# Optimization experiments

Hardware: AMD Instinct MI355X
Metric: run time of the kernel (lower is better)

## Reference

```python
import jax, jax.numpy as jnp
import numpy as np

N_NODES = 100000
N_EDGES = 1600000
NUM_FEATURES = 64
HIDDEN = 64
NUM_CLASSES = 16


def setup_inputs() -> dict:
    key = jax.random.key(0)
    ks = jax.random.split(key, 8)
    x = jax.random.normal(ks[0], (N_NODES, NUM_FEATURES), dtype=jnp.float32)
    edge_index = jax.random.randint(ks[1], (2, N_EDGES), 0, N_NODES, dtype=jnp.int32)
    # Glorot-ish init for weights, zero bias (matches GCNConv / Linear defaults closely enough)
    s1 = 1.0 / np.sqrt(NUM_FEATURES)
    s2 = 1.0 / np.sqrt(HIDDEN)
    W1 = jax.random.uniform(ks[2], (NUM_FEATURES, HIDDEN), jnp.float32, -s1, s1)
    b1 = jnp.zeros((HIDDEN,), jnp.float32)
    W2 = jax.random.uniform(ks[3], (HIDDEN, HIDDEN), jnp.float32, -s2, s2)
    b2 = jnp.zeros((HIDDEN,), jnp.float32)
    W3 = jax.random.uniform(ks[4], (HIDDEN, NUM_CLASSES), jnp.float32, -s2, s2)
    b3 = jax.random.uniform(ks[5], (NUM_CLASSES,), jnp.float32, -s2, s2)
    return {"x": x, "edge_index": edge_index, "W1": W1, "b1": b1,
            "W2": W2, "b2": b2, "W3": W3, "b3": b3}


def _gcn_layer(x, W, b, src, dst, norm, n_nodes):
    # GCNConv: h = X W; out[i] = sum_{(j->i)} norm_ji * h[j]; out += b
    h = x @ W                                   # [N, H] small dense GEMM
    msg = h[src] * norm[:, None]                # [E+N, H] irregular gather
    out = jax.ops.segment_sum(msg, dst, num_segments=n_nodes)  # scatter-add
    return out + b


def reference(x, edge_index, W1, b1, W2, b2, W3, b3):
    n = x.shape[0]
    loop = jnp.arange(n, dtype=edge_index.dtype)
    # add self-loops (PyG GCNConv default add_self_loops=True)
    src = jnp.concatenate([edge_index[0], loop])
    dst = jnp.concatenate([edge_index[1], loop])
    # symmetric normalization D^{-1/2} A_hat D^{-1/2}
    deg = jax.ops.segment_sum(jnp.ones_like(src, dtype=x.dtype), dst, num_segments=n)
    dis = jax.lax.rsqrt(deg)                    # deg >= 1 due to self-loops
    norm = dis[src] * dis[dst]                  # [E+N]

    h = jax.nn.relu(_gcn_layer(x, W1, b1, src, dst, norm, n))
    # F.dropout(training=False) -> identity (module in eval mode)
    h = jax.nn.relu(_gcn_layer(h, W2, b2, src, dst, norm, n))
    z = h @ W3 + b3
    return jax.nn.log_softmax(z, axis=1), h
```

## Files before the change

### kernel.cpp

```cpp
#include <hip/hip_runtime.h>
#include <hip/hip_bf16.h>

typedef __hip_bfloat16 bf16;
typedef unsigned short ushort;

#define NN 100000
#define NE 1600000
#define NBKT 782
#define BCAP 4096
#define EPB 2048
#define NP1 782
#define NMT 6250

typedef __attribute__((ext_vector_type(8))) short s8v;
typedef __attribute__((ext_vector_type(4))) float f4v;

__device__ __forceinline__ float ldf(const void* p, int i, int f32) {
    return f32 ? ((const float*)p)[i] : __bfloat162float(((const bf16*)p)[i]);
}
__device__ __forceinline__ void stf(void* p, int i, int f32, float v) {
    if (f32) ((float*)p)[i] = v;
    else     ((bf16*)p)[i] = __float2bfloat16(v);
}

__device__ __forceinline__ ushort f2b(float f) {
    unsigned u = __builtin_bit_cast(unsigned, f);
    u += 0x7FFF + ((u >> 16) & 1);
    return (ushort)(u >> 16);
}
__device__ __forceinline__ float b2f(ushort h) {
    unsigned u = ((unsigned)h) << 16;
    return __builtin_bit_cast(float, u);
}
__device__ __forceinline__ float blo(unsigned u) {
    return __builtin_bit_cast(float, u << 16);
}
__device__ __forceinline__ float bhi(unsigned u) {
    return __builtin_bit_cast(float, u & 0xffff0000u);
}

__global__ void k_detect(const unsigned* __restrict__ x, int* __restrict__ flag,
                         int* __restrict__ gcur) {
    int gi = blockIdx.x * 256 + threadIdx.x;
    if (gi < 1024) gcur[gi] = 0;
    if (blockIdx.x != 0) return;
    __shared__ int cnt[256];
    int t = threadIdx.x, c = 0;
    for (int i = t; i < 2048; i += 256) {
        unsigned e7 = (x[i] >> 8) & 0x7F;
        c += (e7 >= 60 && e7 <= 66) ? 1 : 0;
    }
    cnt[t] = c;
    __syncthreads();
    for (int s = 128; s > 0; s >>= 1) {
        if (t < s) cnt[t] += cnt[t + s];
        __syncthreads();
    }
    if (t == 0) *flag = (cnt[0] >= 1024) ? 0 : 1;
}

__global__ void k_sentinel(unsigned* out) {
    if (threadIdx.x == 0 && blockIdx.x == 0) out[0] = 0x461C461Cu;
}

__global__ void k_pass1(const int* __restrict__ src, const int* __restrict__ dst,
                        int* __restrict__ gcur, unsigned* __restrict__ bbuf) {
    __shared__ int hist[NBKT];
    __shared__ int base[NBKT];
    int t = threadIdx.x;
    int e0 = blockIdx.x * EPB;
    for (int i = t; i < NBKT; i += 256) hist[i] = 0;
    __syncthreads();
    for (int k = 0; k < EPB; k += 256) {
        int e = e0 + k + t;
        if (e < NE) atomicAdd(&hist[dst[e] >> 7], 1);
    }
    __syncthreads();
    for (int i = t; i < NBKT; i += 256) {
        int c = hist[i];
        base[i] = c ? atomicAdd(&gcur[i], c) : 0;
    }
    __syncthreads();
    for (int i = t; i < NBKT; i += 256) hist[i] = 0;
    __syncthreads();
    for (int k = 0; k < EPB; k += 256) {
        int e = e0 + k + t;
        if (e < NE) {
            int d = dst[e];
            int b = d >> 7;
            int lp = atomicAdd(&hist[b], 1);
            bbuf[b * BCAP + base[b] + lp] = ((unsigned)src[e] << 7) | (unsigned)(d & 127);
        }
    }
}

__global__ void k_scanB(const int* __restrict__ gcur, int* __restrict__ gbase,
                        int* __restrict__ rowptr) {
    __shared__ int s[1024];
    int t = threadIdx.x;
    int v = (t < NBKT) ? gcur[t] : 0;
    s[t] = v;
    __syncthreads();
    for (int d = 1; d < 1024; d <<= 1) {
        int add = (t >= d) ? s[t - d] : 0;
        __syncthreads();
        s[t] += add;
        __syncthreads();
    }
    if (t < NBKT) gbase[t] = s[t] - v;
    if (t == 0) { gbase[NBKT] = NE; rowptr[NN] = NE; }
}

__global__ void k_pass2(const unsigned* __restrict__ bbuf, const int* __restrict__ gbase,
                        int* __restrict__ rowptr, float* __restrict__ dis,
                        int* __restrict__ csr_off) {
    __shared__ unsigned vals[BCAP];
    __shared__ int lout[BCAP];
    __shared__ int fh[128], fx[128], fc[128];
    int b = blockIdx.x, t = threadIdx.x;
    int g0 = gbase[b], cnt = gbase[b + 1] - g0;
    const unsigned* in = bbuf + b * BCAP;
    if (t < 128) fh[t] = 0;
    __syncthreads();
    for (int i = t; i < cnt; i += 256) {
        unsigned v = in[i];
        vals[i] = v;
        atomicAdd(&fh[v & 127], 1);
    }
    __syncthreads();
    if (t < 128) fx[t] = fh[t];
    __syncthreads();
    for (int d = 1; d < 128; d <<= 1) {
        int add = (t >= d && t < 128) ? fx[t - d] : 0;
        __syncthreads();
        if (t < 128) fx[t] += add;
        __syncthreads();
    }
    int n = b * 128 + t;
    if (t < 128) {
        int ex = fx[t] - fh[t];
        fc[t] = ex;
        if (n < NN) {
            rowptr[n] = g0 + ex;
            dis[n] = rsqrtf(1.0f + (float)fh[t]);
        }
    }
    __syncthreads();
    for (int i = t; i < cnt; i += 256) {
        unsigned v = vals[i];
        int p = atomicAdd(&fc[v & 127], 1);
        lout[p] = (int)(v & ~127u);
    }
    __syncthreads();
    for (int i = t; i < cnt; i += 256) csr_off[g0 + i] = lout[i];
}

__global__ void __launch_bounds__(256) k_gemm_mfma(
        const void* __restrict__ A, int aBase, const void* __restrict__ W,
        bf16* __restrict__ C, const float* __restrict__ dis,
        const int* __restrict__ flag) {
    int f32 = *flag;
    int t = threadIdx.x;
    if (blockIdx.x == 0 && t < 64) ((ushort*)C)[NN * 64 + t] = 0;
    int lane = t & 63;
    int w = t >> 6;
    int m = lane & 15, q = lane >> 4;

    s8v bh[2][4], bl[2][4];
#pragma unroll
    for (int st = 0; st < 2; st++)
#pragma unroll
        for (int nt = 0; nt < 4; nt++)
#pragma unroll
            for (int j = 0; j < 8; j++) {
                int k = st * 32 + q * 8 + j;
                float wv = ldf(W, k * 64 + nt * 16 + m, f32);
                ushort h = f2b(wv);
                bh[st][nt][j] = (short)h;
                bl[st][nt][j] = (short)f2b(wv - b2f(h));
            }

    ushort* Cu = (ushort*)C;
    int gw = blockIdx.x * 4 + w;
    int nw = gridDim.x * 4;
    for (int mt = gw; mt < NMT; mt += nw) {
        int row = mt * 16 + m;
        s8v ah[2], al[2];
        if (f32) {
            const float* ap = (const float*)A + aBase + row * 64 + q * 8;
#pragma unroll
            for (int st = 0; st < 2; st++)
#pragma unroll
                for (int j = 0; j < 8; j++) {
                    float v = ap[st * 32 + j];
                    ushort h = f2b(v);
                    ah[st][j] = (short)h;
                    al[st][j] = (short)f2b(v - b2f(h));
                }
        } else {
            const short* ap = (const short*)A + aBase + row * 64 + q * 8;
            ah[0] = *(const s8v*)(ap);
            ah[1] = *(const s8v*)(ap + 32);
        }
        float dr[4];
#pragma unroll
        for (int r = 0; r < 4; r++) dr[r] = dis[mt * 16 + q * 4 + r];
#pragma unroll
        for (int nt = 0; nt < 4; nt++) {
            f4v acc = {0.f, 0.f, 0.f, 0.f};
#pragma unroll
            for (int st = 0; st < 2; st++)
                acc = __builtin_amdgcn_mfma_f32_16x16x32_bf16(ah[st], bh[st][nt], acc, 0, 0, 0);
            if (f32) {
#pragma unroll
                for (int st = 0; st < 2; st++) {
                    acc = __builtin_amdgcn_mfma_f32_16x16x32_bf16(ah[st], bl[st][nt], acc, 0, 0, 0);
                    acc = __builtin_amdgcn_mfma_f32_16x16x32_bf16(al[st], bh[st][nt], acc, 0, 0, 0);
                }
            }
            int col = nt * 16 + m;
#pragma unroll
            for (int r = 0; r < 4; r++) {
                int rr = mt * 16 + q * 4 + r;
                Cu[rr * 64 + col] = f2b(dr[r] * acc[r]);
            }
        }
    }
}

__global__ void __launch_bounds__(256, 4) k_aggregate(
        const bf16* __restrict__ hs, void* hout, int hoBase,
        const float* __restrict__ dis,
        const int* __restrict__ rowptr,
        const int* __restrict__ csr_off,
        const void* __restrict__ bias,
        const int* __restrict__ flag) {
    int f32 = *flag;
    int t = threadIdx.x;
    int n = blockIdx.x * 4 + (t >> 6);
    if (n >= NN) return;
    int l = t & 63;
    int q = l >> 4;
    int m = l & 15;
    int fb = m * 8;
    const char* hb = (const char*)hs;
    int r0 = rowptr[n], r1 = rowptr[n + 1];
    float a0 = 0.f, a1 = 0.f, a2 = 0.f, a3 = 0.f;
    int j = r0;
    for (; j + 16 <= r1; j += 16) {
        int o0 = csr_off[j + q];
        int o1 = csr_off[j + 4 + q];
        int o2 = csr_off[j + 8 + q];
        int o3 = csr_off[j + 12 + q];
        uint2 v0 = *(const uint2*)(hb + o0 + fb);
        uint2 v1 = *(const uint2*)(hb + o1 + fb);
        uint2 v2 = *(const uint2*)(hb + o2 + fb);
        uint2 v3 = *(const uint2*)(hb + o3 + fb);
        a0 += blo(v0.x); a1 += bhi(v0.x); a2 += blo(v0.y); a3 += bhi(v0.y);
        a0 += blo(v1.x); a1 += bhi(v1.x); a2 += blo(v1.y); a3 += bhi(v1.y);
        a0 += blo(v2.x); a1 += bhi(v2.x); a2 += blo(v2.y); a3 += bhi(v2.y);
        a0 += blo(v3.x); a1 += bhi(v3.x); a2 += blo(v3.y); a3 += bhi(v3.y);
    }
    if (j < r1) {
        const int Z = NN * 128;
        int i0 = j + q, i1 = j + 4 + q, i2 = j + 8 + q, i3 = j + 12 + q;
        int o0 = csr_off[i0]; o0 = (i0 < r1) ? o0 : Z;
        int o1 = csr_off[i1]; o1 = (i1 < r1) ? o1 : Z;
        int o2 = csr_off[i2]; o2 = (i2 < r1) ? o2 : Z;
        int o3 = csr_off[i3]; o3 = (i3 < r1) ? o3 : Z;
        uint2 v0 = *(const uint2*)(hb + o0 + fb);
        uint2 v1 = *(const uint2*)(hb + o1 + fb);
        uint2 v2 = *(const uint2*)(hb + o2 + fb);
        uint2 v3 = *(const uint2*)(hb + o3 + fb);
        a0 += blo(v0.x); a1 += bhi(v0.x); a2 += blo(v0.y); a3 += bhi(v0.y);
        a0 += blo(v1.x); a1 += bhi(v1.x); a2 += blo(v1.y); a3 += bhi(v1.y);
        a0 += blo(v2.x); a1 += bhi(v2.x); a2 += blo(v2.y); a3 += bhi(v2.y);
        a0 += blo(v3.x); a1 += bhi(v3.x); a2 += blo(v3.y); a3 += bhi(v3.y);
    }
    a0 += __shfl_xor(a0, 32); a1 += __shfl_xor(a1, 32);
    a2 += __shfl_xor(a2, 32); a3 += __shfl_xor(a3, 32);
    a0 += __shfl_xor(a0, 16); a1 += __shfl_xor(a1, 16);
    a2 += __shfl_xor(a2, 16); a3 += __shfl_xor(a3, 16);
    if (q == 0) {
        uint2 sv = *(const uint2*)(hb + n * 128 + fb);
        float dn = dis[n];
        float b0 = ldf(bias, m * 4 + 0, f32);
        float b1v = ldf(bias, m * 4 + 1, f32);
        float b2v = ldf(bias, m * 4 + 2, f32);
        float b3v = ldf(bias, m * 4 + 3, f32);
        float o0 = fmaxf(dn * (a0 + blo(sv.x)) + b0, 0.f);
        float o1 = fmaxf(dn * (a1 + bhi(sv.x)) + b1v, 0.f);
        float o2 = fmaxf(dn * (a2 + blo(sv.y)) + b2v, 0.f);
        float o3 = fmaxf(dn * (a3 + bhi(sv.y)) + b3v, 0.f);
        if (f32) {
            float4 ov = {o0, o1, o2, o3};
            *(float4*)((float*)hout + hoBase + n * 64 + m * 4) = ov;
        } else {
            unsigned w0 = (unsigned)f2b(o0) | ((unsigned)f2b(o1) << 16);
            unsigned w1 = (unsigned)f2b(o2) | ((unsigned)f2b(o3) << 16);
            uint2 wv; wv.x = w0; wv.y = w1;
            *(uint2*)((ushort*)hout + hoBase + n * 64 + m * 4) = wv;
        }
    }
}

__global__ void k_head(const void* __restrict__ h2, int hBase,
                       const void* __restrict__ W3, const void* __restrict__ b3,
                       void* out, const int* __restrict__ flag) {
    __shared__ float w[64 * 16];
    __shared__ float hrow[16 * 64];
    int f32 = *flag;
    int t = threadIdx.x;
#pragma unroll
    for (int i = 0; i < 4; i++) w[t + i * 256] = ldf(W3, t + i * 256, f32);
    int r0 = blockIdx.x * 16;
#pragma unroll
    for (int i = 0; i < 4; i++) hrow[t + i * 256] = ldf(h2, hBase + r0 * 64 + t + i * 256, f32);
    __syncthreads();
    int lr = t >> 4, c = t & 15;
    float z = ldf(b3, c, f32);
#pragma unroll
    for (int k = 0; k < 64; k++) z += hrow[lr * 64 + k] * w[k * 16 + c];
    float m = z;
#pragma unroll
    for (int off = 8; off >= 1; off >>= 1) m = fmaxf(m, __shfl_xor(m, off, 16));
    float p = expf(z - m);
    float s = p;
#pragma unroll
    for (int off = 8; off >= 1; off >>= 1) s += __shfl_xor(s, off, 16);
    stf(out, (r0 + lr) * 16 + c, f32, z - m - logf(s));
}

extern "C" void kernel_launch(void* const* d_in, const int* in_sizes, int n_in,
                              void* d_out, int out_size, void* d_ws, size_t ws_size,
                              hipStream_t stream) {
    const void* x  = d_in[0];
    const int* ei  = (const int*)d_in[1];
    const void* W1 = d_in[2];
    const void* b1 = d_in[3];
    const void* W2 = d_in[4];
    const void* b2 = d_in[5];
    const void* W3 = d_in[6];
    const void* b3 = d_in[7];

    const size_t NEEDED = (size_t)(1807104 + NBKT * BCAP) * 4;
    if (ws_size < NEEDED) {
        k_sentinel<<<1, 64, 0, stream>>>((unsigned*)d_out);
        return;
    }
    int*      flag    = (int*)d_ws;
    float*    dis     = (float*)d_ws + 256;
    int*      rowptr  = (int*)d_ws + 102656;
    int*      gcur    = (int*)d_ws + 205056;
    int*      gbase   = (int*)d_ws + 206080;
    int*      csr_off = (int*)d_ws + 207104;
    unsigned* bbuf    = (unsigned*)((int*)d_ws + 1807104);
    bf16*     bufA    = (bf16*)bbuf;

    const int* srcp = ei;
    const int* dstp = ei + NE;
    const int HB = NN * 16;

    k_detect<<<4, 256, 0, stream>>>((const unsigned*)x, flag, gcur);

    k_pass1<<<NP1, 256, 0, stream>>>(srcp, dstp, gcur, bbuf);
    k_scanB<<<1, 1024, 0, stream>>>(gcur, gbase, rowptr);
    k_pass2<<<NBKT, 256, 0, stream>>>(bbuf, gbase, rowptr, dis, csr_off);

    k_gemm_mfma<<<512, 256, 0, stream>>>(x, 0, W1, bufA, dis, flag);
    k_aggregate<<<NN / 4, 256, 0, stream>>>(bufA, d_out, HB, dis, rowptr, csr_off, b1, flag);

    k_gemm_mfma<<<512, 256, 0, stream>>>(d_out, HB, W2, bufA, dis, flag);
    k_aggregate<<<NN / 4, 256, 0, stream>>>(bufA, d_out, HB, dis, rowptr, csr_off, b2, flag);

    k_head<<<NN / 16, 256, 0, stream>>>(d_out, HB, W3, b3, d_out, flag);
}
```

Measured before the change: 278.2 us.

## Replace bucketed two-pass CSR build with global atomic histogram, scan, scatter

The CSR build no longer uses the shared-memory bucket sort (bucket histogram, global bucket scan, per-bucket local sort). It now counts per-node degrees with global atomics, prefix-sums them in three small scan kernels, and scatters source offsets with per-node atomic cursors. This removes the 3.2 MB bucket buffer and the per-bucket local sort, but adds more kernel launches and heavy global atomic traffic. The scatter order within each row is also nondeterministic and has less write locality.

```diff
diff --git a/kernel.cpp b/kernel.cpp
--- a/kernel.cpp
+++ b/kernel.cpp
@@ -6,11 +6,8 @@
 
 #define NN 100000
 #define NE 1600000
-#define NBKT 782
-#define BCAP 4096
-#define EPB 2048
-#define NP1 782
 #define NMT 6250
+#define NSC1 98
 
 typedef __attribute__((ext_vector_type(8))) short s8v;
 typedef __attribute__((ext_vector_type(4))) float f4v;
@@ -40,9 +37,9 @@
 }
 
 __global__ void k_detect(const unsigned* __restrict__ x, int* __restrict__ flag,
-                         int* __restrict__ gcur) {
+                         int* __restrict__ deg) {
     int gi = blockIdx.x * 256 + threadIdx.x;
-    if (gi < 1024) gcur[gi] = 0;
+    if (gi < NN) deg[gi] = 0;
     if (blockIdx.x != 0) return;
     __shared__ int cnt[256];
     int t = threadIdx.x, c = 0;
@@ -63,96 +60,87 @@
     if (threadIdx.x == 0 && blockIdx.x == 0) out[0] = 0x461C461Cu;
 }
 
-__global__ void k_pass1(const int* __restrict__ src, const int* __restrict__ dst,
-                        int* __restrict__ gcur, unsigned* __restrict__ bbuf) {
-    __shared__ int hist[NBKT];
-    __shared__ int base[NBKT];
+__global__ void k_hist(const int* __restrict__ dst, int* __restrict__ deg) {
+    int i = blockIdx.x * 256 + threadIdx.x;
+    int stride = gridDim.x * 256;
+    for (int e = i; e < NE; e += stride) atomicAdd(&deg[dst[e]], 1);
+}
+
+__global__ void k_scan1(const int* __restrict__ deg, int* __restrict__ bsum) {
+    __shared__ int s[256];
+    int b = blockIdx.x, t = threadIdx.x;
+    int n0 = b * 1024 + t * 4;
+    int v = 0;
+    if (n0 < NN) {
+        int4 d = *(const int4*)(deg + n0);
+        v = d.x + d.y + d.z + d.w;
+    }
+    s[t] = v;
+    __syncthreads();
+    for (int st = 128; st > 0; st >>= 1) {
+        if (t < st) s[t] += s[t + st];
+        __syncthreads();
+    }
+    if (t == 0) bsum[b] = s[0];
+}
+
+__global__ void k_scan2(int* __restrict__ bsum, int* __restrict__ rowptr) {
+    __shared__ int s[128];
     int t = threadIdx.x;
-    int e0 = blockIdx.x * EPB;
-    for (int i = t; i < NBKT; i += 256) hist[i] = 0;
-    __syncthreads();
-    for (int k = 0; k < EPB; k += 256) {
-        int e = e0 + k + t;
-        if (e < NE) atomicAdd(&hist[dst[e] >> 7], 1);
-    }
-    __syncthreads();
-    for (int i = t; i < NBKT; i += 256) {
-        int c = hist[i];
-        base[i] = c ? atomicAdd(&gcur[i], c) : 0;
-    }
-    __syncthreads();
-    for (int i = t; i < NBKT; i += 256) hist[i] = 0;
-    __syncthreads();
-    for (int k = 0; k < EPB; k += 256) {
-        int e = e0 + k + t;
-        if (e < NE) {
-            int d = dst[e];
-            int b = d >> 7;
-            int lp = atomicAdd(&hist[b], 1);
-            bbuf[b * BCAP + base[b] + lp] = ((unsigned)src[e] << 7) | (unsigned)(d & 127);
-        }
-    }
-}
-
-__global__ void k_scanB(const int* __restrict__ gcur, int* __restrict__ gbase,
-                        int* __restrict__ rowptr) {
-    __shared__ int s[1024];
-    int t = threadIdx.x;
-    int v = (t < NBKT) ? gcur[t] : 0;
+    int v = (t < NSC1) ? bsum[t] : 0;
     s[t] = v;
     __syncthreads();
-    for (int d = 1; d < 1024; d <<= 1) {
+    for (int d = 1; d < 128; d <<= 1) {
         int add = (t >= d) ? s[t - d] : 0;
         __syncthreads();
         s[t] += add;
         __syncthreads();
     }
-    if (t < NBKT) gbase[t] = s[t] - v;
-    if (t == 0) { gbase[NBKT] = NE; rowptr[NN] = NE; }
-}
-
-__global__ void k_pass2(const unsigned* __restrict__ bbuf, const int* __restrict__ gbase,
-                        int* __restrict__ rowptr, float* __restrict__ dis,
-                        int* __restrict__ csr_off) {
-    __shared__ unsigned vals[BCAP];
-    __shared__ int lout[BCAP];
-    __shared__ int fh[128], fx[128], fc[128];
+    if (t < NSC1) bsum[t] = s[t] - v;
+    if (t == 0) rowptr[NN] = NE;
+}
+
+__global__ void k_scan3(int* __restrict__ degcur, const int* __restrict__ bsum,
+                        int* __restrict__ rowptr, float* __restrict__ dis) {
+    __shared__ int s[256];
     int b = blockIdx.x, t = threadIdx.x;
-    int g0 = gbase[b], cnt = gbase[b + 1] - g0;
-    const unsigned* in = bbuf + b * BCAP;
-    if (t < 128) fh[t] = 0;
-    __syncthreads();
-    for (int i = t; i < cnt; i += 256) {
-        unsigned v = in[i];
-        vals[i] = v;
-        atomicAdd(&fh[v & 127], 1);
-    }
-    __syncthreads();
-    if (t < 128) fx[t] = fh[t];
-    __syncthreads();
-    for (int d = 1; d < 128; d <<= 1) {
-        int add = (t >= d && t < 128) ? fx[t - d] : 0;
-        __syncthreads();
-        if (t < 128) fx[t] += add;
-        __syncthreads();
-    }
-    int n = b * 128 + t;
-    if (t < 128) {
-        int ex = fx[t] - fh[t];
-        fc[t] = ex;
-        if (n < NN) {
-            rowptr[n] = g0 + ex;
-            dis[n] = rsqrtf(1.0f + (float)fh[t]);
-        }
-    }
-    __syncthreads();
-    for (int i = t; i < cnt; i += 256) {
-        unsigned v = vals[i];
-        int p = atomicAdd(&fc[v & 127], 1);
-        lout[p] = (int)(v & ~127u);
-    }
-    __syncthreads();
-    for (int i = t; i < cnt; i += 256) csr_off[g0 + i] = lout[i];
+    int n0 = b * 1024 + t * 4;
+    int4 d = {0, 0, 0, 0};
+    if (n0 < NN) d = *(const int4*)(degcur + n0);
+    int sum = d.x + d.y + d.z + d.w;
+    s[t] = sum;
+    __syncthreads();
+    for (int dd = 1; dd < 256; dd <<= 1) {
+        int add = (t >= dd) ? s[t - dd] : 0;
+        __syncthreads();
+        s[t] += add;
+        __syncthreads();
+    }
+    int ex = s[t] - sum + bsum[b];
+    if (n0 < NN) {
+        int r0 = ex;
+        int r1 = r0 + d.x;
+        int r2 = r1 + d.y;
+        int r3 = r2 + d.z;
+        int4 rv = {r0, r1, r2, r3};
+        *(int4*)(rowptr + n0) = rv;
+        float4 dv = {rsqrtf(1.0f + (float)d.x), rsqrtf(1.0f + (float)d.y),
+                     rsqrtf(1.0f + (float)d.z), rsqrtf(1.0f + (float)d.w)};
+        *(float4*)(dis + n0) = dv;
+        *(int4*)(degcur + n0) = rv;
+    }
+}
+
+__global__ void k_scatter(const int* __restrict__ src, const int* __restrict__ dst,
+                          int* __restrict__ cursor, int* __restrict__ csr_off) {
+    int i = blockIdx.x * 256 + threadIdx.x;
+    int stride = gridDim.x * 256;
+    for (int e = i; e < NE; e += stride) {
+        int d = dst[e];
+        int s = src[e];
+        int p = atomicAdd(&cursor[d], 1);
+        csr_off[p] = s << 7;
+    }
 }
 
 __global__ void __launch_bounds__(256) k_gemm_mfma(
@@ -343,7 +331,7 @@
     const void* W3 = d_in[6];
     const void* b3 = d_in[7];
 
-    const size_t NEEDED = (size_t)(1807104 + NBKT * BCAP) * 4;
+    const size_t NEEDED = (size_t)(1807104 + 3203072) * 4;
     if (ws_size < NEEDED) {
         k_sentinel<<<1, 64, 0, stream>>>((unsigned*)d_out);
         return;
@@ -351,21 +339,22 @@
     int*      flag    = (int*)d_ws;
     float*    dis     = (float*)d_ws + 256;
     int*      rowptr  = (int*)d_ws + 102656;
-    int*      gcur    = (int*)d_ws + 205056;
-    int*      gbase   = (int*)d_ws + 206080;
+    int*      bsum    = (int*)d_ws + 205056;
     int*      csr_off = (int*)d_ws + 207104;
-    unsigned* bbuf    = (unsigned*)((int*)d_ws + 1807104);
-    bf16*     bufA    = (bf16*)bbuf;
+    int*      deg     = (int*)d_ws + 1807104;
+    bf16*     bufA    = (bf16*)deg;
 
     const int* srcp = ei;
     const int* dstp = ei + NE;
     const int HB = NN * 16;
 
-    k_detect<<<4, 256, 0, stream>>>((const unsigned*)x, flag, gcur);
-
-    k_pass1<<<NP1, 256, 0, stream>>>(srcp, dstp, gcur, bbuf);
-    k_scanB<<<1, 1024, 0, stream>>>(gcur, gbase, rowptr);
-    k_pass2<<<NBKT, 256, 0, stream>>>(bbuf, gbase, rowptr, dis, csr_off);
+    k_detect<<<(NN + 255) / 256, 256, 0, stream>>>((const unsigned*)x, flag, deg);
+
+    k_hist<<<2048, 256, 0, stream>>>(dstp, deg);
+    k_scan1<<<NSC1, 256, 0, stream>>>(deg, bsum);
+    k_scan2<<<1, 128, 0, stream>>>(bsum, rowptr);
+    k_scan3<<<NSC1, 256, 0, stream>>>(deg, bsum, rowptr, dis);
+    k_scatter<<<2048, 256, 0, stream>>>(srcp, dstp, deg, csr_off);
 
     k_gemm_mfma<<<512, 256, 0, stream>>>(x, 0, W1, bufA, dis, flag);
     k_aggregate<<<NN / 4, 256, 0, stream>>>(bufA, d_out, HB, dis, rowptr, csr_off, b1, flag);
```

After: 437.9 us. 57.4% more time.

## Replace atomic bucket reservation with count/column-scan/place CSR build using 256-node buckets

Applied to the files above, without the earlier changes.

The CSR construction changes from a single pass that reserves bucket space with global atomics into separate kernels: a per-block histogram, a per-bucket column scan over blocks, a bucket-total scan, and a placement pass that writes at deterministic offsets. Buckets grow from 128 to 256 destination nodes and blocks handle twice as many edges, which halves the number of buckets and blocks. The aim is to remove global atomic contention and make edge placement deterministic, at the cost of extra kernel launches and a second read of the dst array.

```diff
diff --git a/kernel.cpp b/kernel.cpp
--- a/kernel.cpp
+++ b/kernel.cpp
@@ -6,10 +6,10 @@
 
 #define NN 100000
 #define NE 1600000
-#define NBKT 782
-#define BCAP 4096
-#define EPB 2048
-#define NP1 782
+#define NBKT 391
+#define BCAP 4608
+#define EPB 4096
+#define NP1 391
 #define NMT 6250
 
 typedef __attribute__((ext_vector_type(8))) short s8v;
@@ -39,11 +39,7 @@
     return __builtin_bit_cast(float, u & 0xffff0000u);
 }
 
-__global__ void k_detect(const unsigned* __restrict__ x, int* __restrict__ flag,
-                         int* __restrict__ gcur) {
-    int gi = blockIdx.x * 256 + threadIdx.x;
-    if (gi < 1024) gcur[gi] = 0;
-    if (blockIdx.x != 0) return;
+__global__ void k_detect(const unsigned* __restrict__ x, int* __restrict__ flag) {
     __shared__ int cnt[256];
     int t = threadIdx.x, c = 0;
     for (int i = t; i < 2048; i += 256) {
@@ -63,52 +59,76 @@
     if (threadIdx.x == 0 && blockIdx.x == 0) out[0] = 0x461C461Cu;
 }
 
-__global__ void k_pass1(const int* __restrict__ src, const int* __restrict__ dst,
-                        int* __restrict__ gcur, unsigned* __restrict__ bbuf) {
+__global__ void k_cnt(const int* __restrict__ dst, int* __restrict__ cnt) {
     __shared__ int hist[NBKT];
-    __shared__ int base[NBKT];
-    int t = threadIdx.x;
-    int e0 = blockIdx.x * EPB;
+    int b = blockIdx.x, t = threadIdx.x;
     for (int i = t; i < NBKT; i += 256) hist[i] = 0;
     __syncthreads();
+    int e0 = b * EPB;
+#pragma unroll
     for (int k = 0; k < EPB; k += 256) {
         int e = e0 + k + t;
-        if (e < NE) atomicAdd(&hist[dst[e] >> 7], 1);
-    }
-    __syncthreads();
+        if (e < NE) atomicAdd(&hist[dst[e] >> 8], 1);
+    }
+    __syncthreads();
+    for (int i = t; i < NBKT; i += 256) cnt[b * NBKT + i] = hist[i];
+}
+
+__global__ void k_colscan(const int* __restrict__ cnt, int* __restrict__ prefT,
+                          int* __restrict__ btot) {
+    __shared__ int s[512];
+    int k = blockIdx.x, t = threadIdx.x;
+    int v = (t < NP1) ? cnt[t * NBKT + k] : 0;
+    s[t] = v;
+    __syncthreads();
+    for (int d = 1; d < 512; d <<= 1) {
+        int add = (t >= d) ? s[t - d] : 0;
+        __syncthreads();
+        s[t] += add;
+        __syncthreads();
+    }
+    if (t < NP1) prefT[k * NP1 + t] = s[t] - v;
+    if (t == 511) btot[k] = s[511];
+}
+
+__global__ void k_scanB(const int* __restrict__ btot, int* __restrict__ gbase,
+                        int* __restrict__ rowptr) {
+    __shared__ int s[512];
+    int t = threadIdx.x;
+    int v = (t < NBKT) ? btot[t] : 0;
+    s[t] = v;
+    __syncthreads();
+    for (int d = 1; d < 512; d <<= 1) {
+        int add = (t >= d) ? s[t - d] : 0;
+        __syncthreads();
+        s[t] += add;
+        __syncthreads();
+    }
+    if (t < NBKT) gbase[t] = s[t] - v;
+    if (t == 0) { gbase[NBKT] = NE; rowptr[NN] = NE; }
+}
+
+__global__ void k_place(const int* __restrict__ src, const int* __restrict__ dst,
+                        const int* __restrict__ prefT, unsigned* __restrict__ bbuf) {
+    __shared__ int base[NBKT];
+    __shared__ int lcur[NBKT];
+    int b = blockIdx.x, t = threadIdx.x;
     for (int i = t; i < NBKT; i += 256) {
-        int c = hist[i];
-        base[i] = c ? atomicAdd(&gcur[i], c) : 0;
-    }
-    __syncthreads();
-    for (int i = t; i < NBKT; i += 256) hist[i] = 0;
-    __syncthreads();
+        base[i] = prefT[i * NP1 + b];
+        lcur[i] = 0;
+    }
+    __syncthreads();
+    int e0 = b * EPB;
+#pragma unroll
     for (int k = 0; k < EPB; k += 256) {
         int e = e0 + k + t;
         if (e < NE) {
             int d = dst[e];
-            int b = d >> 7;
-            int lp = atomicAdd(&hist[b], 1);
-            bbuf[b * BCAP + base[b] + lp] = ((unsigned)src[e] << 7) | (unsigned)(d & 127);
+            int kb = d >> 8;
+            int lp = atomicAdd(&lcur[kb], 1);
+            bbuf[kb * BCAP + base[kb] + lp] = ((unsigned)src[e] << 8) | (unsigned)(d & 255);
         }
     }
-}
-
-__global__ void k_scanB(const int* __restrict__ gcur, int* __restrict__ gbase,
-                        int* __restrict__ rowptr) {
-    __shared__ int s[1024];
-    int t = threadIdx.x;
-    int v = (t < NBKT) ? gcur[t] : 0;
-    s[t] = v;
-    __syncthreads();
-    for (int d = 1; d < 1024; d <<= 1) {
-        int add = (t >= d) ? s[t - d] : 0;
-        __syncthreads();
-        s[t] += add;
-        __syncthreads();
-    }
-    if (t < NBKT) gbase[t] = s[t] - v;
-    if (t == 0) { gbase[NBKT] = NE; rowptr[NN] = NE; }
 }
 
 __global__ void k_pass2(const unsigned* __restrict__ bbuf, const int* __restrict__ gbase,
@@ -116,43 +136,41 @@
                         int* __restrict__ csr_off) {
     __shared__ unsigned vals[BCAP];
     __shared__ int lout[BCAP];
-    __shared__ int fh[128], fx[128], fc[128];
+    __shared__ int fh[256], fx[256], fc[256];
     int b = blockIdx.x, t = threadIdx.x;
-    int g0 = gbase[b], cnt = gbase[b + 1] - g0;
+    int g0 = gbase[b], cntb = gbase[b + 1] - g0;
     const unsigned* in = bbuf + b * BCAP;
-    if (t < 128) fh[t] = 0;
-    __syncthreads();
-    for (int i = t; i < cnt; i += 256) {
+    fh[t] = 0;
+    __syncthreads();
+    for (int i = t; i < cntb; i += 256) {
         unsigned v = in[i];
         vals[i] = v;
-        atomicAdd(&fh[v & 127], 1);
-    }
-    __syncthreads();
-    if (t < 128) fx[t] = fh[t];
-    __syncthreads();
-    for (int d = 1; d < 128; d <<= 1) {
-        int add = (t >= d && t < 128) ? fx[t - d] : 0;
-        __syncthreads();
-        if (t < 128) fx[t] += add;
-        __syncthreads();
-    }
-    int n = b * 128 + t;
-    if (t < 128) {
-        int ex = fx[t] - fh[t];
-        fc[t] = ex;
-        if (n < NN) {
-            rowptr[n] = g0 + ex;
-            dis[n] = rsqrtf(1.0f + (float)fh[t]);
-        }
-    }
-    __syncthreads();
-    for (int i = t; i < cnt; i += 256) {
+        atomicAdd(&fh[v & 255], 1);
+    }
+    __syncthreads();
+    fx[t] = fh[t];
+    __syncthreads();
+    for (int d = 1; d < 256; d <<= 1) {
+        int add = (t >= d) ? fx[t - d] : 0;
+        __syncthreads();
+        fx[t] += add;
+        __syncthreads();
+    }
+    int n = b * 256 + t;
+    int ex = fx[t] - fh[t];
+    fc[t] = ex;
+    if (n < NN) {
+        rowptr[n] = g0 + ex;
+        dis[n] = rsqrtf(1.0f + (float)fh[t]);
+    }
+    __syncthreads();
+    for (int i = t; i < cntb; i += 256) {
         unsigned v = vals[i];
-        int p = atomicAdd(&fc[v & 127], 1);
-        lout[p] = (int)(v & ~127u);
-    }
-    __syncthreads();
-    for (int i = t; i < cnt; i += 256) csr_off[g0 + i] = lout[i];
+        int p = atomicAdd(&fc[v & 255], 1);
+        lout[p] = (int)((v >> 8) << 7);
+    }
+    __syncthreads();
+    for (int i = t; i < cntb; i += 256) csr_off[g0 + i] = lout[i];
 }
 
 __global__ void __launch_bounds__(256) k_gemm_mfma(
@@ -343,7 +361,7 @@
     const void* W3 = d_in[6];
     const void* b3 = d_in[7];
 
-    const size_t NEEDED = (size_t)(1807104 + NBKT * BCAP) * 4;
+    const size_t NEEDED = (size_t)(1807104 + 3203072) * 4;
     if (ws_size < NEEDED) {
         k_sentinel<<<1, 64, 0, stream>>>((unsigned*)d_out);
         return;
@@ -351,20 +369,24 @@
     int*      flag    = (int*)d_ws;
     float*    dis     = (float*)d_ws + 256;
     int*      rowptr  = (int*)d_ws + 102656;
-    int*      gcur    = (int*)d_ws + 205056;
-    int*      gbase   = (int*)d_ws + 206080;
+    int*      gbase   = (int*)d_ws + 205056;
+    int*      btot    = (int*)d_ws + 205568;
     int*      csr_off = (int*)d_ws + 207104;
     unsigned* bbuf    = (unsigned*)((int*)d_ws + 1807104);
+    int*      cnt     = (int*)d_ws + 1807104 + NBKT * BCAP;
+    int*      prefT   = cnt + 153088;
     bf16*     bufA    = (bf16*)bbuf;
 
     const int* srcp = ei;
     const int* dstp = ei + NE;
     const int HB = NN * 16;
 
-    k_detect<<<4, 256, 0, stream>>>((const unsigned*)x, flag, gcur);
-
-    k_pass1<<<NP1, 256, 0, stream>>>(srcp, dstp, gcur, bbuf);
-    k_scanB<<<1, 1024, 0, stream>>>(gcur, gbase, rowptr);
+    k_detect<<<1, 256, 0, stream>>>((const unsigned*)x, flag);
+
+    k_cnt<<<NP1, 256, 0, stream>>>(dstp, cnt);
+    k_colscan<<<NBKT, 512, 0, stream>>>(cnt, prefT, btot);
+    k_scanB<<<1, 512, 0, stream>>>(btot, gbase, rowptr);
+    k_place<<<NP1, 256, 0, stream>>>(srcp, dstp, prefT, bbuf);
     k_pass2<<<NBKT, 256, 0, stream>>>(bbuf, gbase, rowptr, dis, csr_off);
 
     k_gemm_mfma<<<512, 256, 0, stream>>>(x, 0, W1, bufA, dis, flag);
```

Result: faster. 269.4 us (-3.2%).
